# Optimization experiments

Hardware: AMD Instinct MI355X
Metric: run time of the kernel (lower is better)

The kernel has to match this reference:

```python
import math
import jax, jax.numpy as jnp
import numpy as np

NUM_EXPERTS = 8
CAPACITY_FACTOR = 1.5

def setup_inputs() -> dict:
    key = jax.random.key(0)
    ks = jax.random.split(key, 4)
    B, T, D, F, E = 4, 2048, 1024, 4096, NUM_EXPERTS
    scale = 0.02
    return {
        "x": jax.random.normal(ks[0], (B, T, D), dtype=jnp.float32),
        "router_w": jax.random.normal(ks[1], (E, D), dtype=jnp.float32) * scale,  # nn.Linear(D,E,bias=False).weight
        "w1": jax.random.normal(ks[2], (E, D, F), dtype=jnp.float32) * scale,
        "b1": jnp.zeros((E, F), dtype=jnp.float32),
        "w2": jax.random.normal(ks[3], (E, F, D), dtype=jnp.float32) * scale,
        "b2": jnp.zeros((E, D), dtype=jnp.float32),
    }

def reference(x, router_w, w1, b1, w2, b2):
    B, T, D = x.shape
    E = router_w.shape[0]
    N = B * T
    C = max(math.ceil(CAPACITY_FACTOR * N / E), 1)  # static per-expert capacity

    x_flat = x.reshape(N, D)
    logits = x_flat @ router_w.T                      # [N, E]
    probs = jax.nn.softmax(logits, axis=-1)
    chosen_e = jnp.argmax(probs, axis=-1)             # [N] int
    chosen_p = jnp.max(probs, axis=-1)                # [N]

    # First-come-first-served capacity: position of each token within its expert's queue
    onehot = jax.nn.one_hot(chosen_e, E, dtype=jnp.float32)          # [N, E]
    pos = jnp.take_along_axis(jnp.cumsum(onehot, axis=0), chosen_e[:, None], axis=1)[:, 0] - 1.0
    pos = pos.astype(jnp.int32)                                       # [N]
    kept = (pos < C)                                                  # [N] bool
    pos_c = jnp.clip(pos, 0, C - 1)

    # Scatter tokens into per-expert capacity buffers [E, C, D]; dropped tokens contribute 0
    buf = jnp.zeros((E, C, D), dtype=x.dtype).at[chosen_e, pos_c].add(
        x_flat * kept[:, None].astype(x.dtype))

    # Expert FFN: Linear -> exact GELU -> Linear (torch nn.GELU default = erf)
    h = jax.nn.gelu(jnp.einsum('ecd,edf->ecf', buf, w1) + b1[:, None, :], approximate=False)
    eo = jnp.einsum('ecf,efd->ecd', h, w2) + b2[:, None, :]           # [E, C, D]

    # Gather back and scale by router prob; dropped tokens get zeros
    y = eo[chosen_e, pos_c] * (chosen_p * kept.astype(x.dtype))[:, None]
    return y.reshape(B, T, D)
```

## Files before the change

kernel.cpp:

```cpp
#include <hip/hip_runtime.h>
#include <hip/hip_bf16.h>
#include <math.h>

typedef unsigned short u16;
typedef __attribute__((ext_vector_type(8))) short short8;
typedef __attribute__((ext_vector_type(4))) float f32x4;

#define NTOK 8192
#define DMODEL 1024
#define FDIM 4096
#define NEXP 8
#define CAP 1536

__device__ __forceinline__ u16 f2bf(float f) {
  __hip_bfloat16 b = __float2bfloat16(f);
  u16 u;
  __builtin_memcpy(&u, &b, 2);
  return u;
}

__device__ __forceinline__ void gload_lds16(const u16* g, u16* l) {
  __builtin_amdgcn_global_load_lds(
      (const __attribute__((address_space(1))) void*)g,
      (__attribute__((address_space(3))) void*)l, 16, 0, 0);
}

__global__ __launch_bounds__(256) void router_cast_kernel(
    const float* __restrict__ x, const float* __restrict__ rw,
    u16* __restrict__ xbf, int* __restrict__ chosen_e,
    float* __restrict__ chosen_p) {
  int b = blockIdx.x, tid = threadIdx.x;
  if (b < 4096) {
    size_t base = (size_t)b * 2048 + tid * 8;
    float4 v0 = *(const float4*)(x + base);
    float4 v1 = *(const float4*)(x + base + 4);
    short8 sv;
    sv[0] = (short)f2bf(v0.x); sv[1] = (short)f2bf(v0.y);
    sv[2] = (short)f2bf(v0.z); sv[3] = (short)f2bf(v0.w);
    sv[4] = (short)f2bf(v1.x); sv[5] = (short)f2bf(v1.y);
    sv[6] = (short)f2bf(v1.z); sv[7] = (short)f2bf(v1.w);
    *(short8*)(xbf + base) = sv;
  } else {
    int tok = ((b - 4096) * 256 + tid) >> 6;
    int lane = tid & 63;
    const float4* xp = (const float4*)(x + (size_t)tok * DMODEL) + lane * 4;
    float4 x0 = xp[0], x1 = xp[1], x2 = xp[2], x3 = xp[3];
    float l[8];
#pragma unroll
    for (int e = 0; e < 8; e++) {
      const float4* wp = (const float4*)(rw + (size_t)e * DMODEL) + lane * 4;
      float4 w0 = wp[0], w1v = wp[1], w2v = wp[2], w3 = wp[3];
      float s = x0.x * w0.x + x0.y * w0.y + x0.z * w0.z + x0.w * w0.w;
      s += x1.x * w1v.x + x1.y * w1v.y + x1.z * w1v.z + x1.w * w1v.w;
      s += x2.x * w2v.x + x2.y * w2v.y + x2.z * w2v.z + x2.w * w2v.w;
      s += x3.x * w3.x + x3.y * w3.y + x3.z * w3.z + x3.w * w3.w;
      l[e] = s;
    }
#pragma unroll
    for (int off = 32; off > 0; off >>= 1) {
#pragma unroll
      for (int e = 0; e < 8; e++) l[e] += __shfl_xor(l[e], off, 64);
    }
    if (lane == 0) {
      float best = l[0];
      int am = 0;
#pragma unroll
      for (int e = 1; e < 8; e++)
        if (l[e] > best) { best = l[e]; am = e; }
      float denom = 0.f;
#pragma unroll
      for (int e = 0; e < 8; e++) denom += expf(l[e] - best);
      chosen_e[tok] = am;
      chosen_p[tok] = 1.0f / denom;
    }
  }
}

__device__ __forceinline__ void trans256(const float* __restrict__ ip,
                                         u16* __restrict__ op, int Rin,
                                         int Cin, int r0, int c0, char* lds,
                                         int tid) {
  int w = tid >> 6, l = tid & 63;
#pragma unroll
  for (int i = 0; i < 16; i++) {
    int row = w * 16 + i;
    float4 v = *(const float4*)(ip + (size_t)(r0 + row) * Cin + c0 + l * 4);
    uint2 d;
    d.x = (unsigned)f2bf(v.x) | ((unsigned)f2bf(v.y) << 16);
    d.y = (unsigned)f2bf(v.z) | ((unsigned)f2bf(v.w) << 16);
    int ch = (l >> 1) ^ ((row >> 3) & 7);
    *(uint2*)(lds + row * 512 + ch * 16 + (l & 1) * 8) = d;
  }
  __syncthreads();
#pragma unroll
  for (int p = 0; p < 2; p++) {
    int c = ((tid >> 5) + p * 32) * 4;
    int rb = (tid & 31) * 8;
    short8 s0, s1, s2, s3;
#pragma unroll
    for (int j = 0; j < 8; j++) {
      int r = rb + j;
      int ch = (c >> 3) ^ ((r >> 3) & 7);
      uint2 d = *(const uint2*)(lds + r * 512 + ch * 16 + (c & 7) * 2);
      s0[j] = (short)(d.x & 0xffff);
      s1[j] = (short)(d.x >> 16);
      s2[j] = (short)(d.y & 0xffff);
      s3[j] = (short)(d.y >> 16);
    }
    u16* ob = op + (size_t)(c0 + c) * Rin + r0 + rb;
    *(short8*)(ob) = s0;
    *(short8*)(ob + (size_t)Rin) = s1;
    *(short8*)(ob + 2 * (size_t)Rin) = s2;
    *(short8*)(ob + 3 * (size_t)Rin) = s3;
  }
}

__global__ __launch_bounds__(1024, 1) void wtrans_kernel(
    const float* __restrict__ w1, const float* __restrict__ w2,
    u16* __restrict__ w1t, u16* __restrict__ w2t,
    const int* __restrict__ chosen_e, int* __restrict__ tok_of_slot,
    int* __restrict__ counts, float* __restrict__ out) {
  extern __shared__ char lds[];
  int b = blockIdx.x, tid = threadIdx.x;
  if (b == 0) {
    if (tid < 512) {
      int w = tid >> 6, lane = tid & 63;
      unsigned long long ltmask =
          (lane == 63) ? ~0ull >> 1 : (1ull << lane) - 1ull;
      int cnt = 0;
      for (int c = 0; c < NTOK / 64; c++) {
        int i = c * 64 + lane;
        int e = chosen_e[i];
        unsigned long long bal = __ballot(e == w);
        if (e == w) {
          int p = cnt + __popcll(bal & ltmask);
          if (p < CAP) {
            tok_of_slot[w * CAP + p] = i;
          } else {
            float4 z = make_float4(0.f, 0.f, 0.f, 0.f);
            float* orow = out + (size_t)i * DMODEL;
            for (int d = 0; d < DMODEL; d += 4) *(float4*)(orow + d) = z;
          }
        }
        cnt += __popcll(bal);
      }
      for (int p = cnt + lane; p < CAP; p += 64) tok_of_slot[w * CAP + p] = -1;
      if (lane == 0) counts[w] = cnt < CAP ? cnt : CAP;
    }
  } else if (b < 513) {
    int idx = b - 1;
    int e = idx >> 6, rem = idx & 63;
    int r0 = (rem >> 4) * 256, c0 = (rem & 15) * 256;
    trans256(w1 + (size_t)e * DMODEL * FDIM, w1t + (size_t)e * DMODEL * FDIM,
             DMODEL, FDIM, r0, c0, lds, tid);
  } else {
    int idx = b - 513;
    int e = idx >> 6, rem = idx & 63;
    int r0 = (rem >> 2) * 256, c0 = (rem & 3) * 256;
    trans256(w2 + (size_t)e * DMODEL * FDIM, w2t + (size_t)e * DMODEL * FDIM,
             FDIM, DMODEL, r0, c0, lds, tid);
  }
}

template <int NX, int NY>
__device__ __forceinline__ void tile_coords(int& bx, int& by, int& bz) {
  int flat = blockIdx.x + NX * (blockIdx.y + NY * blockIdx.z);
  int nwg = NX * NY * (int)gridDim.z;
  int swz = (flat & 7) * (nwg >> 3) + (flat >> 3);
  bx = swz % NX;
  int rem = swz / NX;
  by = rem % NY;
  bz = rem / NY;
}

template <int KD>
__device__ __forceinline__ void mainloop_db(const u16* pa0, const u16* pa1,
                                            const u16* pb0, const u16* pb1,
                                            u16* smem, f32x4 (&acc)[4][4],
                                            int tid) {
  int wid = tid >> 6, lane = tid & 63;
  int wm = (wid >> 1) * 64, wn = (wid & 1) * 64;
  int fr = lane & 15, fk = (lane >> 4) * 8;
  int aro = (wm + fr) * 32 + fk;
  int bro = 4096 + (wn + fr) * 32 + fk;
  gload_lds16(pa0, smem + tid * 8);
  gload_lds16(pa1, smem + 2048 + tid * 8);
  gload_lds16(pb0, smem + 4096 + tid * 8);
  gload_lds16(pb1, smem + 6144 + tid * 8);
  __syncthreads();
  int cur = 0;
#pragma unroll 1
  for (int t = 0; t < KD / 32; ++t) {
    const u16* cb = smem + cur * 8192;
    u16* nb = smem + (cur ^ 1) * 8192;
    if (t + 1 < KD / 32) {
      int k = (t + 1) * 32;
      gload_lds16(pa0 + k, nb + tid * 8);
      gload_lds16(pa1 + k, nb + 2048 + tid * 8);
      gload_lds16(pb0 + k, nb + 4096 + tid * 8);
      gload_lds16(pb1 + k, nb + 6144 + tid * 8);
    }
    short8 av[4], bv[4];
#pragma unroll
    for (int m = 0; m < 4; m++) av[m] = *(const short8*)(cb + aro + m * 512);
#pragma unroll
    for (int n = 0; n < 4; n++) bv[n] = *(const short8*)(cb + bro + n * 512);
#pragma unroll
    for (int m = 0; m < 4; m++)
#pragma unroll
      for (int n = 0; n < 4; n++)
        acc[m][n] = __builtin_amdgcn_mfma_f32_16x16x32_bf16(av[m], bv[n],
                                                            acc[m][n], 0, 0, 0);
    __syncthreads();
    cur ^= 1;
  }
}

template <int NX, int NY>
__global__ __launch_bounds__(512) void gemm1_kernel(
    const u16* __restrict__ xbf, const u16* __restrict__ w1tB,
    const int* __restrict__ tok_of_slot, const int* __restrict__ counts,
    u16* __restrict__ hB, const float* __restrict__ b1, int e0,
    long long hStrideE) {
  extern __shared__ __align__(16) u16 smem[];
  int bx, by, bz;
  tile_coords<NX, NY>(bx, by, bz);
  int e = e0 + bz;
  int m0 = by * 128, n0 = bx * 256;
  if (m0 >= counts[e]) return;
  const u16* Bg = w1tB + (size_t)e * FDIM * DMODEL;
  u16* H = hB + (size_t)bz * hStrideE;
  const float* b1g = b1 + (size_t)e * FDIM;
  int tid = threadIdx.x;
  int r2 = tid >> 2, c8 = (tid & 3) * 8;
  int t0 = tok_of_slot[e * CAP + m0 + r2];
  t0 &= ~(t0 >> 31);
  const u16* pa0 = xbf + (size_t)t0 * DMODEL + c8;
  const u16* pb0 = Bg + (size_t)(n0 + r2) * DMODEL + c8;
  const u16* pb1 = pb0 + (size_t)128 * DMODEL;
  f32x4 acc[4][4] = {};
  {
    int wid = tid >> 6, lane = tid & 63;
    int wm = (wid >> 2) * 64, wn = (wid & 3) * 64;
    int fr = lane & 15, fk = (lane >> 4) * 8;
    int aro = (wm + fr) * 32 + fk;
    int bro = 4096 + (wn + fr) * 32 + fk;
    gload_lds16(pa0, smem + tid * 8);
    gload_lds16(pb0, smem + 4096 + tid * 8);
    gload_lds16(pb1, smem + 8192 + tid * 8);
    __syncthreads();
    int cur = 0;
#pragma unroll 1
    for (int t = 0; t < DMODEL / 32; ++t) {
      const u16* cb = smem + cur * 12288;
      u16* nb = smem + (cur ^ 1) * 12288;
      if (t + 1 < DMODEL / 32) {
        int k = (t + 1) * 32;
        gload_lds16(pa0 + k, nb + tid * 8);
        gload_lds16(pb0 + k, nb + 4096 + tid * 8);
        gload_lds16(pb1 + k, nb + 8192 + tid * 8);
      }
      short8 av[4], bv[4];
#pragma unroll
      for (int m = 0; m < 4; m++) av[m] = *(const short8*)(cb + aro + m * 512);
#pragma unroll
      for (int n = 0; n < 4; n++) bv[n] = *(const short8*)(cb + bro + n * 512);
#pragma unroll
      for (int m = 0; m < 4; m++)
#pragma unroll
        for (int n = 0; n < 4; n++)
          acc[m][n] = __builtin_amdgcn_mfma_f32_16x16x32_bf16(
              av[m], bv[n], acc[m][n], 0, 0, 0);
      __syncthreads();
      cur ^= 1;
    }
  }
  int wid = tid >> 6, lane = tid & 63;
  int wm = (wid >> 2) * 64, wn = (wid & 3) * 64;
  int fr = lane & 15, fq = lane >> 4;
  float bias[4];
#pragma unroll
  for (int n = 0; n < 4; n++) bias[n] = b1g[n0 + wn + n * 16 + fr];
#pragma unroll
  for (int m = 0; m < 4; m++) {
#pragma unroll
    for (int n = 0; n < 4; n++) {
      int colL = wn + n * 16 + fr;
#pragma unroll
      for (int j = 0; j < 4; j++) {
        int rL = wm + m * 16 + fq * 4 + j;
        float v = acc[m][n][j] + bias[n];
        v = 0.5f * v * (1.0f + erff(v * 0.70710678118654752f));
        int ch = (colL >> 3) ^ ((rL >> 2) & 7);
        smem[rL * 256 + ch * 8 + (colL & 7)] = f2bf(v);
      }
    }
  }
  __syncthreads();
#pragma unroll
  for (int p = 0; p < 8; p++) {
    int rr = p * 16 + (tid >> 5);
    int cch = tid & 31;
    int ch = cch ^ ((rr >> 2) & 7);
    short8 v = *(const short8*)(smem + rr * 256 + ch * 8);
    *(short8*)(H + (size_t)(m0 + rr) * FDIM + n0 + cch * 8) = v;
  }
}

template <int NX, int NY>
__global__ __launch_bounds__(256) void gemm2_kernel(
    const u16* __restrict__ hB, const u16* __restrict__ w2tB,
    float* __restrict__ out, const float* __restrict__ b2,
    const int* __restrict__ tok_of_slot, const int* __restrict__ counts,
    const float* __restrict__ chosen_p, int e0, long long hStrideE) {
  __shared__ __align__(16) u16 smem[16384];
  int bx, by, bz;
  tile_coords<NX, NY>(bx, by, bz);
  int e = e0 + bz;
  int m0 = by * 128, n0 = bx * 128;
  if (m0 >= counts[e]) return;
  const u16* Ag = hB + (size_t)bz * hStrideE;
  const u16* Bg = w2tB + (size_t)e * DMODEL * FDIM;
  const float* b2g = b2 + (size_t)e * DMODEL;
  int tid = threadIdx.x;
  int r2 = tid >> 2, c8 = (tid & 3) * 8;
  const u16* pa0 = Ag + (size_t)(m0 + r2) * FDIM + c8;
  const u16* pa1 = pa0 + (size_t)64 * FDIM;
  const u16* pb0 = Bg + (size_t)(n0 + r2) * FDIM + c8;
  const u16* pb1 = pb0 + (size_t)64 * FDIM;
  f32x4 acc[4][4] = {};
  mainloop_db<FDIM>(pa0, pa1, pb0, pb1, smem, acc, tid);

  int wid = tid >> 6, lane = tid & 63;
  int wm = (wid >> 1) * 64, wn = (wid & 1) * 64;
  int fr = lane & 15, fq = lane >> 4;
  float bias[4];
#pragma unroll
  for (int n = 0; n < 4; n++) bias[n] = b2g[n0 + wn + n * 16 + fr];
#pragma unroll
  for (int m = 0; m < 4; m++) {
#pragma unroll
    for (int j = 0; j < 4; j++) {
      int rL = wm + m * 16 + fq * 4 + j;
      int tk = tok_of_slot[e * CAP + m0 + rL];
      if (tk >= 0) {
        float sc = chosen_p[tk];
#pragma unroll
        for (int n = 0; n < 4; n++) {
          int colL = wn + n * 16 + fr;
          out[(size_t)tk * DMODEL + n0 + colL] = (acc[m][n][j] + bias[n]) * sc;
        }
      }
    }
  }
}

extern "C" void kernel_launch(void* const* d_in, const int* in_sizes, int n_in,
                              void* d_out, int out_size, void* d_ws,
                              size_t ws_size, hipStream_t stream) {
  const float* x = (const float*)d_in[0];
  const float* rw = (const float*)d_in[1];
  const float* w1 = (const float*)d_in[2];
  const float* b1 = (const float*)d_in[3];
  const float* w2 = (const float*)d_in[4];
  const float* b2 = (const float*)d_in[5];
  float* out = (float*)d_out;

  char* ws = (char*)d_ws;
  size_t off = 0;
  auto alloc = [&](size_t bytes) -> void* {
    void* p = ws + off;
    off = (off + bytes + 255) & ~(size_t)255;
    return p;
  };
  int* chosen_e = (int*)alloc((size_t)NTOK * 4);
  float* chosen_p = (float*)alloc((size_t)NTOK * 4);
  int* tok_of_slot = (int*)alloc((size_t)NEXP * CAP * 4);
  int* counts = (int*)alloc(NEXP * 4);
  u16* xbf = (u16*)alloc((size_t)NTOK * DMODEL * 2);
  u16* w1t = (u16*)alloc((size_t)NEXP * DMODEL * FDIM * 2);
  u16* w2t = (u16*)alloc((size_t)NEXP * DMODEL * FDIM * 2);
  size_t hFull = (size_t)NEXP * CAP * FDIM * 2;
  size_t hLoop = (size_t)CAP * FDIM * 2;
  bool full = (off + hFull) <= ws_size;
  u16* h = (u16*)alloc(full ? hFull : hLoop);

  static_assert(CAP % 128 == 0 && FDIM % 256 == 0 && DMODEL % 128 == 0, "");
  const int TLDS = 131072, G1LDS = 65536;
  hipFuncSetAttribute((const void*)wtrans_kernel,
                      hipFuncAttributeMaxDynamicSharedMemorySize, TLDS);
  hipFuncSetAttribute((const void*)gemm1_kernel<FDIM / 256, CAP / 128>,
                      hipFuncAttributeMaxDynamicSharedMemorySize, G1LDS);

  router_cast_kernel<<<4096 + NTOK / 4, 256, 0, stream>>>(x, rw, xbf, chosen_e,
                                                          chosen_p);
  wtrans_kernel<<<1025, 1024, TLDS, stream>>>(w1, w2, w1t, w2t, chosen_e,
                                              tok_of_slot, counts, out);

  if (full) {
    gemm1_kernel<FDIM / 256, CAP / 128>
        <<<dim3(FDIM / 256, CAP / 128, NEXP), 512, G1LDS, stream>>>(
            xbf, w1t, tok_of_slot, counts, h, b1, 0, (long long)CAP * FDIM);
    gemm2_kernel<DMODEL / 128, CAP / 128>
        <<<dim3(DMODEL / 128, CAP / 128, NEXP), 256, 0, stream>>>(
            h, w2t, out, b2, tok_of_slot, counts, chosen_p, 0,
            (long long)CAP * FDIM);
  } else {
    for (int e = 0; e < NEXP; e++) {
      gemm1_kernel<FDIM / 256, CAP / 128>
          <<<dim3(FDIM / 256, CAP / 128, 1), 512, G1LDS, stream>>>(
              xbf, w1t, tok_of_slot, counts, h, b1, e, 0);
      gemm2_kernel<DMODEL / 128, CAP / 128>
          <<<dim3(DMODEL / 128, CAP / 128, 1), 256, 0, stream>>>(
              h, w2t, out, b2, tok_of_slot, counts, chosen_p, e, 0);
    }
  }
  (void)in_sizes;
  (void)n_in;
  (void)ws_size;
}
```

Before: 333.2 us.

## Restructure gemm1 into 256x256 tiles with 4-stage LDS pipeline and fast GELU

The first expert GEMM moves from 128x256 to 256x256 output tiles, so each wave computes 128x64 with an 8x4 accumulator array. The K loop now uses a four-buffer LDS ring with three tiles of global_load_lds prefetch in flight. MFMA bursts are split into halves separated by explicit barriers, vmcnt waits and setprio raises, so loads overlap with compute. The erff-based GELU is replaced with the Abramowitz-Stegun polynomial using a fast reciprocal and exp. The tradeoff is 128KB of LDS per block and more accumulator registers, which may reduce occupancy, plus a small change in GELU accuracy.

Measured after the change: 333.3 us. About the same (+0.0%).

```diff
diff --git a/kernel.cpp b/kernel.cpp
--- a/kernel.cpp
+++ b/kernel.cpp
@@ -17,6 +17,19 @@
   u16 u;
   __builtin_memcpy(&u, &b, 2);
   return u;
+}
+
+__device__ __forceinline__ float gelu_exact(float v) {
+  float x = v * 0.70710678118654752f;
+  float ax = fabsf(x);
+  float t = __builtin_amdgcn_rcpf(1.0f + 0.3275911f * ax);
+  float p =
+      t * (0.254829592f +
+           t * (-0.284496736f +
+                t * (1.421413741f + t * (-1.453152027f + t * 1.061405429f))));
+  float er = 1.0f - p * __expf(-ax * ax);
+  er = copysignf(er, x);
+  return 0.5f * v * (1.0f + er);
 }
 
 __device__ __forceinline__ void gload_lds16(const u16* g, u16* l) {
@@ -216,8 +229,65 @@
   }
 }
 
+#define VMWAIT(N) asm volatile("s_waitcnt vmcnt(" #N ")" ::: "memory")
+#define LGKM0 asm volatile("s_waitcnt lgkmcnt(0)" ::: "memory")
+
+#define G1_STAGE_A(t)                                              \
+  {                                                                \
+    u16* d_ = smem + ((t) & 3) * 16384 + tid * 8;                  \
+    gload_lds16(pa0 + (t) * 32, d_);                               \
+    gload_lds16(pa1 + (t) * 32, d_ + 4096);                        \
+  }
+#define G1_STAGE_B(t)                                              \
+  {                                                                \
+    u16* d_ = smem + ((t) & 3) * 16384 + 8192 + tid * 8;           \
+    gload_lds16(pb0 + (t) * 32, d_);                               \
+    gload_lds16(pb1 + (t) * 32, d_ + 4096);                        \
+  }
+
+#define G1_TILE(t, VMSTMT, DO_ISSUE)                                          \
+  {                                                                           \
+    const u16* Ab_ = smem + ((t) & 3) * 16384;                                \
+    short8 a_[8], b0_, b1_;                                                   \
+    _Pragma("unroll") for (int m_ = 0; m_ < 8; m_++) a_[m_] =                 \
+        *(const short8*)(Ab_ + aoff + m_ * 512);                              \
+    b0_ = *(const short8*)(Ab_ + boff);                                       \
+    b1_ = *(const short8*)(Ab_ + boff + 512);                                 \
+    if (DO_ISSUE) G1_STAGE_A((t) + 3);                                        \
+    __builtin_amdgcn_s_barrier();                                             \
+    LGKM0;                                                                    \
+    __builtin_amdgcn_s_setprio(1);                                            \
+    _Pragma("unroll") for (int m_ = 0; m_ < 8; m_++) {                        \
+      acc[m_][0] = __builtin_amdgcn_mfma_f32_16x16x32_bf16(a_[m_], b0_,       \
+                                                           acc[m_][0], 0, 0,  \
+                                                           0);                \
+      acc[m_][1] = __builtin_amdgcn_mfma_f32_16x16x32_bf16(a_[m_], b1_,       \
+                                                           acc[m_][1], 0, 0,  \
+                                                           0);                \
+    }                                                                         \
+    __builtin_amdgcn_s_setprio(0);                                            \
+    __builtin_amdgcn_s_barrier();                                             \
+    short8 b2_ = *(const short8*)(Ab_ + boff + 1024);                         \
+    short8 b3_ = *(const short8*)(Ab_ + boff + 1536);                         \
+    if (DO_ISSUE) G1_STAGE_B((t) + 3);                                        \
+    VMSTMT;                                                                   \
+    __builtin_amdgcn_s_barrier();                                             \
+    LGKM0;                                                                    \
+    __builtin_amdgcn_s_setprio(1);                                            \
+    _Pragma("unroll") for (int m_ = 0; m_ < 8; m_++) {                        \
+      acc[m_][2] = __builtin_amdgcn_mfma_f32_16x16x32_bf16(a_[m_], b2_,       \
+                                                           acc[m_][2], 0, 0,  \
+                                                           0);                \
+      acc[m_][3] = __builtin_amdgcn_mfma_f32_16x16x32_bf16(a_[m_], b3_,       \
+                                                           acc[m_][3], 0, 0,  \
+                                                           0);                \
+    }                                                                         \
+    __builtin_amdgcn_s_setprio(0);                                            \
+    __builtin_amdgcn_s_barrier();                                             \
+  }
+
 template <int NX, int NY>
-__global__ __launch_bounds__(512) void gemm1_kernel(
+__global__ __launch_bounds__(512, 2) void gemm1_kernel(
     const u16* __restrict__ xbf, const u16* __restrict__ w1tB,
     const int* __restrict__ tok_of_slot, const int* __restrict__ counts,
     u16* __restrict__ hB, const float* __restrict__ b1, int e0,
@@ -226,71 +296,56 @@
   int bx, by, bz;
   tile_coords<NX, NY>(bx, by, bz);
   int e = e0 + bz;
-  int m0 = by * 128, n0 = bx * 256;
+  int m0 = by * 256, n0 = bx * 256;
   if (m0 >= counts[e]) return;
   const u16* Bg = w1tB + (size_t)e * FDIM * DMODEL;
   u16* H = hB + (size_t)bz * hStrideE;
-  const float* b1g = b1 + (size_t)e * FDIM;
   int tid = threadIdx.x;
-  int r2 = tid >> 2, c8 = (tid & 3) * 8;
-  int t0 = tok_of_slot[e * CAP + m0 + r2];
+
+  int r4 = tid >> 2, c8 = (tid & 3) * 8;
+  int t0 = tok_of_slot[e * CAP + m0 + r4];
   t0 &= ~(t0 >> 31);
+  int t1 = tok_of_slot[e * CAP + m0 + 128 + r4];
+  t1 &= ~(t1 >> 31);
   const u16* pa0 = xbf + (size_t)t0 * DMODEL + c8;
-  const u16* pb0 = Bg + (size_t)(n0 + r2) * DMODEL + c8;
+  const u16* pa1 = xbf + (size_t)t1 * DMODEL + c8;
+  const u16* pb0 = Bg + (size_t)(n0 + r4) * DMODEL + c8;
   const u16* pb1 = pb0 + (size_t)128 * DMODEL;
-  f32x4 acc[4][4] = {};
-  {
-    int wid = tid >> 6, lane = tid & 63;
-    int wm = (wid >> 2) * 64, wn = (wid & 3) * 64;
-    int fr = lane & 15, fk = (lane >> 4) * 8;
-    int aro = (wm + fr) * 32 + fk;
-    int bro = 4096 + (wn + fr) * 32 + fk;
-    gload_lds16(pa0, smem + tid * 8);
-    gload_lds16(pb0, smem + 4096 + tid * 8);
-    gload_lds16(pb1, smem + 8192 + tid * 8);
-    __syncthreads();
-    int cur = 0;
+
+  int wid = tid >> 6, lane = tid & 63;
+  int wm = (wid >> 2) * 128, wn = (wid & 3) * 64;
+  int fr = lane & 15, fk = (lane >> 4) * 8;
+  int aoff = (wm + fr) * 32 + fk;
+  int boff = 8192 + (wn + fr) * 32 + fk;
+  f32x4 acc[8][4] = {};
+
+  G1_STAGE_A(0); G1_STAGE_B(0);
+  G1_STAGE_A(1); G1_STAGE_B(1);
+  G1_STAGE_A(2); G1_STAGE_B(2);
+  VMWAIT(8);
+  __builtin_amdgcn_s_barrier();
+
+  const int KT = DMODEL / 32;
 #pragma unroll 1
-    for (int t = 0; t < DMODEL / 32; ++t) {
-      const u16* cb = smem + cur * 12288;
-      u16* nb = smem + (cur ^ 1) * 12288;
-      if (t + 1 < DMODEL / 32) {
-        int k = (t + 1) * 32;
-        gload_lds16(pa0 + k, nb + tid * 8);
-        gload_lds16(pb0 + k, nb + 4096 + tid * 8);
-        gload_lds16(pb1 + k, nb + 8192 + tid * 8);
-      }
-      short8 av[4], bv[4];
-#pragma unroll
-      for (int m = 0; m < 4; m++) av[m] = *(const short8*)(cb + aro + m * 512);
-#pragma unroll
-      for (int n = 0; n < 4; n++) bv[n] = *(const short8*)(cb + bro + n * 512);
-#pragma unroll
-      for (int m = 0; m < 4; m++)
-#pragma unroll
-        for (int n = 0; n < 4; n++)
-          acc[m][n] = __builtin_amdgcn_mfma_f32_16x16x32_bf16(
-              av[m], bv[n], acc[m][n], 0, 0, 0);
-      __syncthreads();
-      cur ^= 1;
-    }
-  }
-  int wid = tid >> 6, lane = tid & 63;
-  int wm = (wid >> 2) * 64, wn = (wid & 3) * 64;
-  int fr = lane & 15, fq = lane >> 4;
+  for (int t = 0; t < KT - 3; ++t) G1_TILE(t, VMWAIT(8), true);
+  G1_TILE(KT - 3, VMWAIT(4), false);
+  G1_TILE(KT - 2, VMWAIT(0), false);
+  G1_TILE(KT - 1, (void)0, false);
+
+  int fq = lane >> 4;
+  const float* b1g = b1 + (size_t)e * FDIM + n0;
   float bias[4];
 #pragma unroll
-  for (int n = 0; n < 4; n++) bias[n] = b1g[n0 + wn + n * 16 + fr];
-#pragma unroll
-  for (int m = 0; m < 4; m++) {
+  for (int n = 0; n < 4; n++) bias[n] = b1g[wn + n * 16 + fr];
+#pragma unroll
+  for (int m = 0; m < 8; m++) {
 #pragma unroll
     for (int n = 0; n < 4; n++) {
       int colL = wn + n * 16 + fr;
 #pragma unroll
       for (int j = 0; j < 4; j++) {
         int rL = wm + m * 16 + fq * 4 + j;
-        float v = acc[m][n][j] + bias[n];
-        v = 0.5f * v * (1.0f + erff(v * 0.70710678118654752f));
+        float v = gelu_exact(acc[m][n][j] + bias[n]);
         int ch = (colL >> 3) ^ ((rL >> 2) & 7);
         smem[rL * 256 + ch * 8 + (colL & 7)] = f2bf(v);
       }
@@ -298,9 +353,9 @@
   }
   __syncthreads();
 #pragma unroll
-  for (int p = 0; p < 8; p++) {
-    int rr = p * 16 + (tid >> 5);
-    int cch = tid & 31;
+  for (int p = 0; p < 16; p++) {
+    int idx = p * 512 + tid;
+    int rr = idx >> 5, cch = idx & 31;
     int ch = cch ^ ((rr >> 2) & 7);
     short8 v = *(const short8*)(smem + rr * 256 + ch * 8);
     *(short8*)(H + (size_t)(m0 + rr) * FDIM + n0 + cch * 8) = v;
@@ -385,11 +440,11 @@
   bool full = (off + hFull) <= ws_size;
   u16* h = (u16*)alloc(full ? hFull : hLoop);
 
-  static_assert(CAP % 128 == 0 && FDIM % 256 == 0 && DMODEL % 128 == 0, "");
-  const int TLDS = 131072, G1LDS = 65536;
+  static_assert(CAP % 256 == 0 && FDIM % 256 == 0 && DMODEL % 128 == 0, "");
+  const int TLDS = 131072, G1LDS = 131072;
   hipFuncSetAttribute((const void*)wtrans_kernel,
                       hipFuncAttributeMaxDynamicSharedMemorySize, TLDS);
-  hipFuncSetAttribute((const void*)gemm1_kernel<FDIM / 256, CAP / 128>,
+  hipFuncSetAttribute((const void*)gemm1_kernel<FDIM / 256, CAP / 256>,
                       hipFuncAttributeMaxDynamicSharedMemorySize, G1LDS);
 
   router_cast_kernel<<<4096 + NTOK / 4, 256, 0, stream>>>(x, rw, xbf, chosen_e,
@@ -398,8 +453,8 @@
                                               tok_of_slot, counts, out);
 
   if (full) {
-    gemm1_kernel<FDIM / 256, CAP / 128>
-        <<<dim3(FDIM / 256, CAP / 128, NEXP), 512, G1LDS, stream>>>(
+    gemm1_kernel<FDIM / 256, CAP / 256>
+        <<<dim3(FDIM / 256, CAP / 256, NEXP), 512, G1LDS, stream>>>(
             xbf, w1t, tok_of_slot, counts, h, b1, 0, (long long)CAP * FDIM);
     gemm2_kernel<DMODEL / 128, CAP / 128>
         <<<dim3(DMODEL / 128, CAP / 128, NEXP), 256, 0, stream>>>(
@@ -407,8 +462,8 @@
             (long long)CAP * FDIM);
   } else {
     for (int e = 0; e < NEXP; e++) {
-      gemm1_kernel<FDIM / 256, CAP / 128>
-          <<<dim3(FDIM / 256, CAP / 128, 1), 512, G1LDS, stream>>>(
+      gemm1_kernel<FDIM / 256, CAP / 256>
+          <<<dim3(FDIM / 256, CAP / 256, 1), 512, G1LDS, stream>>>(
               xbf, w1t, tok_of_slot, counts, h, b1, e, 0);
       gemm2_kernel<DMODEL / 128, CAP / 128>
           <<<dim3(DMODEL / 128, CAP / 128, 1), 256, 0, stream>>>(
```
